# Optimization experiments

Measured on AMD Instinct MI355X. Metric: run time of the kernel, lower is better.

Reference implementation:

```python
import jax, jax.numpy as jnp
import numpy as np

B, T, NIN, H = 256, 100, 64, 1024


def _lstm_cell(x, h, c, Wih, Whh, bih, bhh):
    # torch.nn.LSTMCell: gates = x@Wih^T + bih + h@Whh^T + bhh, order (i, f, g, o)
    gates = x @ Wih.T + bih + h @ Whh.T + bhh  # [B, 4H]
    i, f, g, o = jnp.split(gates, 4, axis=-1)
    i = jax.nn.sigmoid(i)
    f = jax.nn.sigmoid(f)
    g = jnp.tanh(g)
    o = jax.nn.sigmoid(o)
    c_new = f * c + i * g
    h_new = o * jnp.tanh(c_new)
    return h_new, c_new


def setup_inputs() -> dict:
    key = jax.random.key(0)
    ks = jax.random.split(key, 17)
    s_in = 1.0 / np.sqrt(H)
    d = {"x": jax.random.normal(ks[0], (B, T, NIN), dtype=jnp.float32)}
    dims_in = [NIN, H, H, H]
    ki = 1
    for layer in range(1, 5):
        din = dims_in[layer - 1]
        d[f"Wih{layer}"] = jax.random.normal(ks[ki], (4 * H, din), dtype=jnp.float32) * s_in; ki += 1
        d[f"Whh{layer}"] = jax.random.normal(ks[ki], (4 * H, H), dtype=jnp.float32) * s_in; ki += 1
        d[f"bih{layer}"] = jax.random.normal(ks[ki], (4 * H,), dtype=jnp.float32) * s_in; ki += 1
        d[f"bhh{layer}"] = jax.random.normal(ks[ki], (4 * H,), dtype=jnp.float32) * s_in; ki += 1
        ks = jax.random.split(ks[-1], 17)
        ki = 0
    return d


def reference(x, Wih1, Whh1, bih1, bhh1, Wih2, Whh2, bih2, bhh2,
              Wih3, Whh3, bih3, bhh3, Wih4, Whh4, bih4, bhh4):
    batch = x.shape[0]
    params = ((Wih1, Whh1, bih1, bhh1), (Wih2, Whh2, bih2, bhh2),
              (Wih3, Whh3, bih3, bhh3), (Wih4, Whh4, bih4, bhh4))
    zeros = jnp.zeros((batch, H), dtype=x.dtype)
    init = tuple((zeros, zeros) for _ in range(4))

    def step(carry, xt):
        new_carry = []
        inp = xt
        for (h, c), (Wih, Whh, bih, bhh) in zip(carry, params):
            h, c = _lstm_cell(inp, h, c, Wih, Whh, bih, bhh)
            new_carry.append((h, c))
            inp = h
        return tuple(new_carry), inp  # top-layer h

    xs = jnp.swapaxes(x, 0, 1)  # [T, B, NIN]
    carry, hs = jax.lax.scan(step, init, xs)
    out = jnp.swapaxes(hs, 0, 1)  # [B, T, H]
    c4 = carry[3][1]
    return out, c4
```

## Files before the change

### kernel.cpp

```cpp
#include <hip/hip_runtime.h>
#include <hip/hip_bf16.h>

typedef __hip_bfloat16 bf16;
typedef unsigned short u16;
typedef unsigned int u32;
typedef __attribute__((ext_vector_type(8))) short bf16x8;
typedef __attribute__((ext_vector_type(4))) float f32x4;

#define BATCH 256
#define TLEN 100
#define HDIM 1024
#define G4 4096
#define OUT_HT (BATCH * TLEN * HDIM)

#define WS_WP 0u
#define WS_BIAS 59244544u
#define WS_XT 59310080u
#define WS_H 62586880u
#define WS_BAR (WS_H + 4194304u)

__device__ __forceinline__ float sigm(float x) { return 1.0f / (1.0f + __expf(-x)); }
__device__ __forceinline__ float tanh_(float x) { return 2.0f / (1.0f + __expf(-2.0f * x)) - 1.0f; }

__device__ __forceinline__ void gl_lds16(const void* g, void* l) {
  __builtin_amdgcn_global_load_lds((const __attribute__((address_space(1))) u32*)g,
                                   (__attribute__((address_space(3))) u32*)l, 16, 0, 0);
}

__device__ __forceinline__ void gbar(u32* arrive, u32* release, u32 epoch, int tid) {
  __syncthreads();
  if (tid == 0) {
    u32 old = __hip_atomic_fetch_add(arrive, 1u, __ATOMIC_ACQ_REL, __HIP_MEMORY_SCOPE_AGENT);
    if (old == 255u) {
      __hip_atomic_store(arrive, 0u, __ATOMIC_RELAXED, __HIP_MEMORY_SCOPE_AGENT);
      __hip_atomic_store(release, epoch, __ATOMIC_RELEASE, __HIP_MEMORY_SCOPE_AGENT);
    } else {
      while (__hip_atomic_load(release, __ATOMIC_RELAXED, __HIP_MEMORY_SCOPE_AGENT) < epoch)
        __builtin_amdgcn_s_sleep(2);
      __builtin_amdgcn_fence(__ATOMIC_ACQUIRE, "agent");
    }
  }
  __syncthreads();
}


__global__ void pack_w(const float* __restrict__ wih, const float* __restrict__ whh,
                       bf16* __restrict__ dst, int NC, int din) {
  int i = blockIdx.x * 256 + threadIdx.x;
  if (i >= 32 * NC * 128 * 64) return;
  int k6 = i & 63;
  int r = (i >> 6) & 127;
  int jc = i >> 13;
  int c = jc % NC;
  int j = jc / NC;
  int grow = ((r >> 5) << 10) + j * 32 + (r & 31);
  int k = c * 64 + k6;
  float v = (k < din) ? wih[grow * din + k] : whh[(grow << 10) + (k - din)];
  dst[(jc << 13) + (r << 6) + (k6 ^ ((r & 7) << 3))] = __float2bfloat16(v);
}

__global__ void pack_bias(const float* __restrict__ a, const float* __restrict__ b,
                          float* __restrict__ dst) {
  int i = blockIdx.x * 256 + threadIdx.x;
  if (i < G4) dst[i] = a[i] + b[i];
}

__global__ void pack_x(const float* __restrict__ x, bf16* __restrict__ xT) {
  int i = blockIdx.x * 256 + threadIdx.x;
  if (i >= TLEN * BATCH * 64) return;
  int k = i & 63;
  int b = (i >> 6) & 255;
  int t = i >> 14;
  xT[(t << 14) + (b << 6) + (k ^ ((b & 7) << 3))] = __float2bfloat16(x[(b * TLEN + t) * 64 + k]);
}


__global__ void __launch_bounds__(512, 2)
lstm_main(const u16* __restrict__ Wp, const float* __restrict__ biasc,
          const u16* __restrict__ xT, u16* __restrict__ hbuf,
          float* __restrict__ out, u32* __restrict__ barr) {
  __shared__ __align__(16) u16 smem[73728];

  const int tid = threadIdx.x;
  const int lane = tid & 63;
  const int wave = tid >> 6;
  const int wg = blockIdx.x;
  const int layer = wg >> 6;
  const int sub = wg & 63;
  const int b0 = (sub >> 5) * 128;
  const int h0 = (sub & 31) * 32;

  const int NC = (layer == 0) ? 17 : 32;
  const int T0 = (layer == 0) ? 1 : 16;
  const u16* Wsl = Wp + ((layer == 0) ? 0u : (4456448u + (u32)(layer - 1) * 8388608u))
                 + (u32)(sub & 31) * (u32)NC * 8192u;

  const int nn = tid & 31;
  float bias_r[4];
#pragma unroll
  for (int g = 0; g < 4; ++g) bias_r[g] = biasc[layer * G4 + g * HDIM + h0 + nn];

  const int r0 = (tid >> 5) * 8;
  float cst[8];
#pragma unroll
  for (int k = 0; k < 8; ++k) cst[k] = 0.0f;

  const int opu0 = (wave * 2) * 512 + lane * 8;
  const int opu1 = opu0 + 512;

  const int mh = (wave >> 2) & 1;
  const int nh = (wave >> 1) & 1;
  const int kh = wave & 1;
  const int lrow = lane & 15;
  const int lswz = (lane & 7) << 4;
  const int kbyte = kh * 64 + ((lane >> 4) << 4);
  const int kx = kbyte ^ lswz;

  float* G0 = (float*)smem;
  float* G1 = (float*)((char*)smem + 67584);

  u32* bar_arrive = barr;
  u32* bar_release = barr + 32;

  for (int s = 0; s < TLEN + 3; ++s) {
    const int t = s - layer;
    if (t >= 0 && t < TLEN) {
      const u16* aBase0 = ((layer == 0) ? (xT + (u32)t * 16384u)
                                        : (hbuf + (u32)((layer - 1) * 2 + (t & 1)) * 262144u))
                        + b0 * 64;
      const u16* aBase1 = hbuf + (u32)(layer * 2 + ((t + 1) & 1)) * 262144u + b0 * 64;

      f32x4 acc[4][4];
#pragma unroll
      for (int mt = 0; mt < 4; ++mt)
#pragma unroll
        for (int nt = 0; nt < 4; ++nt) acc[mt][nt] = (f32x4)(0.0f);

      auto issueA = [&](int c, int slot) {
        const u16* src = (c < T0) ? (aBase0 + c * 16384) : (aBase1 + (c - T0) * 16384);
        gl_lds16(src + opu0, smem + slot * 8192 + (wave * 2) * 512);
        gl_lds16(src + opu1, smem + slot * 8192 + (wave * 2 + 1) * 512);
      };
      auto issueB = [&](int c, int slot) {
        const u16* src = Wsl + c * 8192;
        gl_lds16(src + opu0, smem + 32768 + slot * 8192 + (wave * 2) * 512);
        gl_lds16(src + opu1, smem + 32768 + slot * 8192 + (wave * 2 + 1) * 512);
      };

      issueB(0, 0);
      issueB(1, 1);
      issueA(0, 0); issueB(2, 2);
      issueA(1, 1); issueB(3, 3);

      for (int c = 0; c < NC; ++c) {
        {
          int ca = c + 2; int cca = (ca < NC) ? ca : (NC - 1);
          issueA(cca, ca & 3);
          int cb = c + 4; int ccb = (cb < NC) ? cb : (NC - 1);
          issueB(ccb, cb % 5);
        }
        asm volatile("s_waitcnt vmcnt(10)" ::: "memory");
        __builtin_amdgcn_s_barrier();

        const char* Abuf = (const char*)smem + (c & 3) * 16384;
        const char* Bbuf = (const char*)smem + 65536 + (c % 5) * 16384;
        bf16x8 a[4], b[4];
#pragma unroll
        for (int mt = 0; mt < 4; ++mt) {
          int row = mh * 64 + mt * 16 + lrow;
          a[mt] = *(const bf16x8*)(Abuf + row * 128 + kx);
        }
#pragma unroll
        for (int nt = 0; nt < 4; ++nt) {
          int row = nh * 64 + nt * 16 + lrow;
          b[nt] = *(const bf16x8*)(Bbuf + row * 128 + kx);
        }
#pragma unroll
        for (int mt = 0; mt < 4; ++mt)
#pragma unroll
          for (int nt = 0; nt < 4; ++nt)
            acc[mt][nt] = __builtin_amdgcn_mfma_f32_16x16x32_bf16(a[mt], b[nt], acc[mt][nt], 0, 0, 0);

        __builtin_amdgcn_s_barrier();
      }

      asm volatile("s_waitcnt vmcnt(0)" ::: "memory");
      __syncthreads();

      float* Gw = kh ? G1 : G0;
#pragma unroll
      for (int mt = 0; mt < 4; ++mt)
#pragma unroll
        for (int nt = 0; nt < 4; ++nt) {
          int row = mh * 64 + mt * 16 + (lane >> 4) * 4;
          int col = nh * 64 + nt * 16 + (lane & 15);
#pragma unroll
          for (int r = 0; r < 4; ++r) Gw[(row + r) * 132 + col] = acc[mt][nt][r];
        }
      __syncthreads();

      u16* outSlot = hbuf + (u32)(layer * 2 + (t & 1)) * 262144u;
      const int hcol = h0 + nn;
      const int j2 = hcol >> 6;
      const int colin = hcol & 63;
#pragma unroll
      for (int k = 0; k < 8; ++k) {
        int r = r0 + k;
        float gi = G0[r * 132 + nn]      + G1[r * 132 + nn]      + bias_r[0];
        float gf = G0[r * 132 + 32 + nn] + G1[r * 132 + 32 + nn] + bias_r[1];
        float gg = G0[r * 132 + 64 + nn] + G1[r * 132 + 64 + nn] + bias_r[2];
        float go = G0[r * 132 + 96 + nn] + G1[r * 132 + 96 + nn] + bias_r[3];
        float iv = sigm(gi), fv = sigm(gf), gv = tanh_(gg), ov = sigm(go);
        float cv = fv * cst[k] + iv * gv;
        cst[k] = cv;
        float hv = ov * tanh_(cv);
        int b = b0 + r;
        bf16 hb = __float2bfloat16(hv);
        outSlot[j2 * 16384 + b * 64 + (colin ^ ((b & 7) << 3))] = *(u16*)&hb;
        if (layer == 3) {
          out[((size_t)b * TLEN + t) * HDIM + hcol] = hv;
          if (t == TLEN - 1) out[OUT_HT + (size_t)b * HDIM + hcol] = cv;
        }
      }
    }
    if (s < TLEN + 2) gbar(bar_arrive, bar_release, (u32)(s + 1), tid);
  }
}


extern "C" void kernel_launch(void* const* d_in, const int* in_sizes, int n_in,
                              void* d_out, int out_size, void* d_ws, size_t ws_size,
                              hipStream_t stream) {
  const float* x = (const float*)d_in[0];
  const float* Wih[4] = {(const float*)d_in[1], (const float*)d_in[5],
                         (const float*)d_in[9], (const float*)d_in[13]};
  const float* Whh[4] = {(const float*)d_in[2], (const float*)d_in[6],
                         (const float*)d_in[10], (const float*)d_in[14]};
  const float* bih[4] = {(const float*)d_in[3], (const float*)d_in[7],
                         (const float*)d_in[11], (const float*)d_in[15]};
  const float* bhh[4] = {(const float*)d_in[4], (const float*)d_in[8],
                         (const float*)d_in[12], (const float*)d_in[16]};

  char* ws = (char*)d_ws;
  bf16* Wp = (bf16*)(ws + WS_WP);
  float* biasc = (float*)(ws + WS_BIAS);
  bf16* xT = (bf16*)(ws + WS_XT);
  u16* hbuf = (u16*)(ws + WS_H);
  u32* barr = (u32*)(ws + WS_BAR);
  float* out = (float*)d_out;

  for (int l = 0; l < 4; ++l) {
    int NC = (l == 0) ? 17 : 32;
    int din = (l == 0) ? 64 : 1024;
    bf16* dst = Wp + ((l == 0) ? 0 : (4456448 + (size_t)(l - 1) * 8388608));
    int total = 32 * NC * 128 * 64;
    pack_w<<<(total + 255) / 256, 256, 0, stream>>>(Wih[l], Whh[l], dst, NC, din);
    pack_bias<<<16, 256, 0, stream>>>(bih[l], bhh[l], biasc + l * 4096);
  }
  pack_x<<<(TLEN * BATCH * 64 + 255) / 256, 256, 0, stream>>>(x, xT);
  hipMemsetAsync(ws + WS_H, 0, 4194304u + 256u, stream);

  void* args[] = {(void*)&Wp, (void*)&biasc, (void*)&xT, (void*)&hbuf, (void*)&out, (void*)&barr};
  hipLaunchCooperativeKernel((void*)lstm_main, dim3(256), dim3(512), args, 0, stream);
}
```

Baseline: 3.274 ms.

## Replace global grid barrier with per-block dataflow flags for wavefront LSTM

Swaps the all-256-block barrier after each diagonal step for per-workgroup progress flags. Each block waits only on the blocks it depends on: the layer below at the current timestep, its own layer's previous h, and the layer above (for the double-buffer reuse hazard), all within its batch half. This lets blocks run ahead instead of synchronising on the slowest block in the grid. The cost is more polling loads, plus correctness that depends on the double-buffer reuse conditions being exactly right.

Result: faster. 3.166 ms (-3.3%).

```diff
diff --git a/kernel.cpp b/kernel.cpp
--- a/kernel.cpp
+++ b/kernel.cpp
@@ -17,7 +17,7 @@
 #define WS_BIAS 59244544u
 #define WS_XT 59310080u
 #define WS_H 62586880u
-#define WS_BAR (WS_H + 4194304u)
+#define WS_FLAGS (WS_H + 4194304u)
 
 __device__ __forceinline__ float sigm(float x) { return 1.0f / (1.0f + __expf(-x)); }
 __device__ __forceinline__ float tanh_(float x) { return 2.0f / (1.0f + __expf(-2.0f * x)) - 1.0f; }
@@ -25,22 +25,6 @@
 __device__ __forceinline__ void gl_lds16(const void* g, void* l) {
   __builtin_amdgcn_global_load_lds((const __attribute__((address_space(1))) u32*)g,
                                    (__attribute__((address_space(3))) u32*)l, 16, 0, 0);
-}
-
-__device__ __forceinline__ void gbar(u32* arrive, u32* release, u32 epoch, int tid) {
-  __syncthreads();
-  if (tid == 0) {
-    u32 old = __hip_atomic_fetch_add(arrive, 1u, __ATOMIC_ACQ_REL, __HIP_MEMORY_SCOPE_AGENT);
-    if (old == 255u) {
-      __hip_atomic_store(arrive, 0u, __ATOMIC_RELAXED, __HIP_MEMORY_SCOPE_AGENT);
-      __hip_atomic_store(release, epoch, __ATOMIC_RELEASE, __HIP_MEMORY_SCOPE_AGENT);
-    } else {
-      while (__hip_atomic_load(release, __ATOMIC_RELAXED, __HIP_MEMORY_SCOPE_AGENT) < epoch)
-        __builtin_amdgcn_s_sleep(2);
-      __builtin_amdgcn_fence(__ATOMIC_ACQUIRE, "agent");
-    }
-  }
-  __syncthreads();
 }
 
 
@@ -78,7 +62,7 @@
 __global__ void __launch_bounds__(512, 2)
 lstm_main(const u16* __restrict__ Wp, const float* __restrict__ biasc,
           const u16* __restrict__ xT, u16* __restrict__ hbuf,
-          float* __restrict__ out, u32* __restrict__ barr) {
+          float* __restrict__ out, u32* __restrict__ flags) {
   __shared__ __align__(16) u16 smem[73728];
 
   const int tid = threadIdx.x;
@@ -87,7 +71,8 @@
   const int wg = blockIdx.x;
   const int layer = wg >> 6;
   const int sub = wg & 63;
-  const int b0 = (sub >> 5) * 128;
+  const int bt = sub >> 5;
+  const int b0 = bt * 128;
   const int h0 = (sub & 31) * 32;
 
   const int NC = (layer == 0) ? 17 : 32;
@@ -119,111 +104,130 @@
   float* G0 = (float*)smem;
   float* G1 = (float*)((char*)smem + 67584);
 
-  u32* bar_arrive = barr;
-  u32* bar_release = barr + 32;
-
-  for (int s = 0; s < TLEN + 3; ++s) {
-    const int t = s - layer;
-    if (t >= 0 && t < TLEN) {
-      const u16* aBase0 = ((layer == 0) ? (xT + (u32)t * 16384u)
-                                        : (hbuf + (u32)((layer - 1) * 2 + (t & 1)) * 262144u))
-                        + b0 * 64;
-      const u16* aBase1 = hbuf + (u32)(layer * 2 + ((t + 1) & 1)) * 262144u + b0 * 64;
-
-      f32x4 acc[4][4];
+  u32* myflag = flags + (layer * 2 + bt) * 32 + (sub & 31);
+  const u32 jj = lane & 31;
+  const u32* pPrev = flags + (((layer > 0 ? layer - 1 : 0) * 2 + bt) * 32) + jj;
+  const u32* pNext = flags + (((layer < 3 ? layer + 1 : 3) * 2 + bt) * 32) + jj;
+  const u32* pOwn  = flags + ((layer * 2 + bt) * 32) + jj;
+
+  for (int t = 0; t < TLEN; ++t) {
+    if (wave == 0) {
+      const bool needP = (layer > 0) && (lane < 32);
+      const bool needN = (layer < 3) && (lane < 32) && (t >= 2);
+      const bool needO = (lane >= 32) && (t >= 1);
+      while (true) {
+        bool ok = true;
+        if (needP) ok &= (__hip_atomic_load(pPrev, __ATOMIC_RELAXED, __HIP_MEMORY_SCOPE_AGENT) >= (u32)(t + 1));
+        if (needN) ok &= (__hip_atomic_load(pNext, __ATOMIC_RELAXED, __HIP_MEMORY_SCOPE_AGENT) >= (u32)(t - 1));
+        if (needO) ok &= (__hip_atomic_load(pOwn,  __ATOMIC_RELAXED, __HIP_MEMORY_SCOPE_AGENT) >= (u32)t);
+        if (__all(ok)) break;
+        __builtin_amdgcn_s_sleep(1);
+      }
+      __builtin_amdgcn_fence(__ATOMIC_ACQUIRE, "agent");
+    }
+    __syncthreads();
+
+    const u16* aBase0 = ((layer == 0) ? (xT + (u32)t * 16384u)
+                                      : (hbuf + (u32)((layer - 1) * 2 + (t & 1)) * 262144u))
+                      + b0 * 64;
+    const u16* aBase1 = hbuf + (u32)(layer * 2 + ((t + 1) & 1)) * 262144u + b0 * 64;
+
+    f32x4 acc[4][4];
+#pragma unroll
+    for (int mt = 0; mt < 4; ++mt)
+#pragma unroll
+      for (int nt = 0; nt < 4; ++nt) acc[mt][nt] = (f32x4)(0.0f);
+
+    auto issueA = [&](int c, int slot) {
+      const u16* src = (c < T0) ? (aBase0 + c * 16384) : (aBase1 + (c - T0) * 16384);
+      gl_lds16(src + opu0, smem + slot * 8192 + (wave * 2) * 512);
+      gl_lds16(src + opu1, smem + slot * 8192 + (wave * 2 + 1) * 512);
+    };
+    auto issueB = [&](int c, int slot) {
+      const u16* src = Wsl + c * 8192;
+      gl_lds16(src + opu0, smem + 32768 + slot * 8192 + (wave * 2) * 512);
+      gl_lds16(src + opu1, smem + 32768 + slot * 8192 + (wave * 2 + 1) * 512);
+    };
+
+    issueB(0, 0);
+    issueB(1, 1);
+    issueA(0, 0); issueB(2, 2);
+    issueA(1, 1); issueB(3, 3);
+
+    for (int c = 0; c < NC; ++c) {
+      {
+        int ca = c + 2; int cca = (ca < NC) ? ca : (NC - 1);
+        issueA(cca, ca & 3);
+        int cb = c + 4; int ccb = (cb < NC) ? cb : (NC - 1);
+        issueB(ccb, cb % 5);
+      }
+      asm volatile("s_waitcnt vmcnt(10)" ::: "memory");
+      __builtin_amdgcn_s_barrier();
+
+      const char* Abuf = (const char*)smem + (c & 3) * 16384;
+      const char* Bbuf = (const char*)smem + 65536 + (c % 5) * 16384;
+      bf16x8 a[4], b[4];
+#pragma unroll
+      for (int mt = 0; mt < 4; ++mt) {
+        int row = mh * 64 + mt * 16 + lrow;
+        a[mt] = *(const bf16x8*)(Abuf + row * 128 + kx);
+      }
+#pragma unroll
+      for (int nt = 0; nt < 4; ++nt) {
+        int row = nh * 64 + nt * 16 + lrow;
+        b[nt] = *(const bf16x8*)(Bbuf + row * 128 + kx);
+      }
 #pragma unroll
       for (int mt = 0; mt < 4; ++mt)
 #pragma unroll
-        for (int nt = 0; nt < 4; ++nt) acc[mt][nt] = (f32x4)(0.0f);
-
-      auto issueA = [&](int c, int slot) {
-        const u16* src = (c < T0) ? (aBase0 + c * 16384) : (aBase1 + (c - T0) * 16384);
-        gl_lds16(src + opu0, smem + slot * 8192 + (wave * 2) * 512);
-        gl_lds16(src + opu1, smem + slot * 8192 + (wave * 2 + 1) * 512);
-      };
-      auto issueB = [&](int c, int slot) {
-        const u16* src = Wsl + c * 8192;
-        gl_lds16(src + opu0, smem + 32768 + slot * 8192 + (wave * 2) * 512);
-        gl_lds16(src + opu1, smem + 32768 + slot * 8192 + (wave * 2 + 1) * 512);
-      };
-
-      issueB(0, 0);
-      issueB(1, 1);
-      issueA(0, 0); issueB(2, 2);
-      issueA(1, 1); issueB(3, 3);
-
-      for (int c = 0; c < NC; ++c) {
-        {
-          int ca = c + 2; int cca = (ca < NC) ? ca : (NC - 1);
-          issueA(cca, ca & 3);
-          int cb = c + 4; int ccb = (cb < NC) ? cb : (NC - 1);
-          issueB(ccb, cb % 5);
-        }
-        asm volatile("s_waitcnt vmcnt(10)" ::: "memory");
-        __builtin_amdgcn_s_barrier();
-
-        const char* Abuf = (const char*)smem + (c & 3) * 16384;
-        const char* Bbuf = (const char*)smem + 65536 + (c % 5) * 16384;
-        bf16x8 a[4], b[4];
-#pragma unroll
-        for (int mt = 0; mt < 4; ++mt) {
-          int row = mh * 64 + mt * 16 + lrow;
-          a[mt] = *(const bf16x8*)(Abuf + row * 128 + kx);
-        }
-#pragma unroll
-        for (int nt = 0; nt < 4; ++nt) {
-          int row = nh * 64 + nt * 16 + lrow;
-          b[nt] = *(const bf16x8*)(Bbuf + row * 128 + kx);
-        }
-#pragma unroll
-        for (int mt = 0; mt < 4; ++mt)
-#pragma unroll
-          for (int nt = 0; nt < 4; ++nt)
-            acc[mt][nt] = __builtin_amdgcn_mfma_f32_16x16x32_bf16(a[mt], b[nt], acc[mt][nt], 0, 0, 0);
-
-        __builtin_amdgcn_s_barrier();
-      }
-
-      asm volatile("s_waitcnt vmcnt(0)" ::: "memory");
-      __syncthreads();
-
-      float* Gw = kh ? G1 : G0;
-#pragma unroll
-      for (int mt = 0; mt < 4; ++mt)
-#pragma unroll
-        for (int nt = 0; nt < 4; ++nt) {
-          int row = mh * 64 + mt * 16 + (lane >> 4) * 4;
-          int col = nh * 64 + nt * 16 + (lane & 15);
-#pragma unroll
-          for (int r = 0; r < 4; ++r) Gw[(row + r) * 132 + col] = acc[mt][nt][r];
-        }
-      __syncthreads();
-
-      u16* outSlot = hbuf + (u32)(layer * 2 + (t & 1)) * 262144u;
-      const int hcol = h0 + nn;
-      const int j2 = hcol >> 6;
-      const int colin = hcol & 63;
-#pragma unroll
-      for (int k = 0; k < 8; ++k) {
-        int r = r0 + k;
-        float gi = G0[r * 132 + nn]      + G1[r * 132 + nn]      + bias_r[0];
-        float gf = G0[r * 132 + 32 + nn] + G1[r * 132 + 32 + nn] + bias_r[1];
-        float gg = G0[r * 132 + 64 + nn] + G1[r * 132 + 64 + nn] + bias_r[2];
-        float go = G0[r * 132 + 96 + nn] + G1[r * 132 + 96 + nn] + bias_r[3];
-        float iv = sigm(gi), fv = sigm(gf), gv = tanh_(gg), ov = sigm(go);
-        float cv = fv * cst[k] + iv * gv;
-        cst[k] = cv;
-        float hv = ov * tanh_(cv);
-        int b = b0 + r;
-        bf16 hb = __float2bfloat16(hv);
-        outSlot[j2 * 16384 + b * 64 + (colin ^ ((b & 7) << 3))] = *(u16*)&hb;
-        if (layer == 3) {
-          out[((size_t)b * TLEN + t) * HDIM + hcol] = hv;
-          if (t == TLEN - 1) out[OUT_HT + (size_t)b * HDIM + hcol] = cv;
-        }
-      }
+        for (int nt = 0; nt < 4; ++nt)
+          acc[mt][nt] = __builtin_amdgcn_mfma_f32_16x16x32_bf16(a[mt], b[nt], acc[mt][nt], 0, 0, 0);
+
+      __builtin_amdgcn_s_barrier();
     }
-    if (s < TLEN + 2) gbar(bar_arrive, bar_release, (u32)(s + 1), tid);
+
+    asm volatile("s_waitcnt vmcnt(0)" ::: "memory");
+    __syncthreads();
+
+    float* Gw = kh ? G1 : G0;
+#pragma unroll
+    for (int mt = 0; mt < 4; ++mt)
+#pragma unroll
+      for (int nt = 0; nt < 4; ++nt) {
+        int row = mh * 64 + mt * 16 + (lane >> 4) * 4;
+        int col = nh * 64 + nt * 16 + (lane & 15);
+#pragma unroll
+        for (int r = 0; r < 4; ++r) Gw[(row + r) * 132 + col] = acc[mt][nt][r];
+      }
+    __syncthreads();
+
+    u16* outSlot = hbuf + (u32)(layer * 2 + (t & 1)) * 262144u;
+    const int hcol = h0 + nn;
+    const int j2 = hcol >> 6;
+    const int colin = hcol & 63;
+#pragma unroll
+    for (int k = 0; k < 8; ++k) {
+      int r = r0 + k;
+      float gi = G0[r * 132 + nn]      + G1[r * 132 + nn]      + bias_r[0];
+      float gf = G0[r * 132 + 32 + nn] + G1[r * 132 + 32 + nn] + bias_r[1];
+      float gg = G0[r * 132 + 64 + nn] + G1[r * 132 + 64 + nn] + bias_r[2];
+      float go = G0[r * 132 + 96 + nn] + G1[r * 132 + 96 + nn] + bias_r[3];
+      float iv = sigm(gi), fv = sigm(gf), gv = tanh_(gg), ov = sigm(go);
+      float cv = fv * cst[k] + iv * gv;
+      cst[k] = cv;
+      float hv = ov * tanh_(cv);
+      int b = b0 + r;
+      bf16 hb = __float2bfloat16(hv);
+      outSlot[j2 * 16384 + b * 64 + (colin ^ ((b & 7) << 3))] = *(u16*)&hb;
+      if (layer == 3) {
+        out[((size_t)b * TLEN + t) * HDIM + hcol] = hv;
+        if (t == TLEN - 1) out[OUT_HT + (size_t)b * HDIM + hcol] = cv;
+      }
+    }
+
+    __syncthreads();
+    if (tid == 0)
+      __hip_atomic_store(myflag, (u32)(t + 1), __ATOMIC_RELEASE, __HIP_MEMORY_SCOPE_AGENT);
   }
 }
 
@@ -246,7 +250,7 @@
   float* biasc = (float*)(ws + WS_BIAS);
   bf16* xT = (bf16*)(ws + WS_XT);
   u16* hbuf = (u16*)(ws + WS_H);
-  u32* barr = (u32*)(ws + WS_BAR);
+  u32* flags = (u32*)(ws + WS_FLAGS);
   float* out = (float*)d_out;
 
   for (int l = 0; l < 4; ++l) {
@@ -258,8 +262,8 @@
     pack_bias<<<16, 256, 0, stream>>>(bih[l], bhh[l], biasc + l * 4096);
   }
   pack_x<<<(TLEN * BATCH * 64 + 255) / 256, 256, 0, stream>>>(x, xT);
-  hipMemsetAsync(ws + WS_H, 0, 4194304u + 256u, stream);
-
-  void* args[] = {(void*)&Wp, (void*)&biasc, (void*)&xT, (void*)&hbuf, (void*)&out, (void*)&barr};
+  hipMemsetAsync(ws + WS_H, 0, 4194304u + 1024u, stream);
+
+  void* args[] = {(void*)&Wp, (void*)&biasc, (void*)&xT, (void*)&hbuf, (void*)&out, (void*)&flags};
   hipLaunchCooperativeKernel((void*)lstm_main, dim3(256), dim3(512), args, 0, stream);
 }
```
